# Kernel tuning notes

Hardware: AMD Instinct MI355X
Metric: run time of the kernel (lower is better)

## Reference

```python
import jax, jax.numpy as jnp
import numpy as np

COMPRESSION = 2  # max-pool factor along flattened spatial axis for phi and g


def setup_inputs() -> dict:
    key = jax.random.key(0)
    ks = jax.random.split(key, 5)
    B, C, H, W = 4, 64, 96, 96
    Ci = 32  # intermediate_dim = C // 2
    s = 1.0 / np.sqrt(C)
    return {
        "x": jax.random.normal(ks[0], (B, C, H, W), dtype=jnp.float32),
        "w_theta": jax.random.normal(ks[1], (Ci, C), dtype=jnp.float32) * s,
        "b_theta": jnp.zeros((Ci,), dtype=jnp.float32),
        "w_phi": jax.random.normal(ks[2], (Ci, C), dtype=jnp.float32) * s,
        "b_phi": jnp.zeros((Ci,), dtype=jnp.float32),
        "w_g": jax.random.normal(ks[3], (Ci, C), dtype=jnp.float32) * s,
        "b_g": jnp.zeros((Ci,), dtype=jnp.float32),
        "w_out": jax.random.normal(ks[4], (C, Ci), dtype=jnp.float32) * (1.0 / np.sqrt(Ci)),
        "b_out": jnp.zeros((C,), dtype=jnp.float32),
    }


def reference(x, w_theta, b_theta, w_phi, b_phi, w_g, b_g, w_out, b_out):
    B, C, H, W = x.shape
    N = H * W
    xf = x.reshape(B, C, N).transpose(0, 2, 1)            # [B, N, C]
    # 1x1 conv projections == channel matmuls
    theta = xf @ w_theta.T + b_theta                      # [B, N, Ci]
    phi = xf @ w_phi.T + b_phi                            # [B, N, Ci]
    g = xf @ w_g.T + b_g                                  # [B, N, Ci]
    # compression: max-pool (kernel=stride=COMPRESSION) along flattened spatial axis
    Ci = theta.shape[-1]
    phi = phi.reshape(B, N // COMPRESSION, COMPRESSION, Ci).max(axis=2)  # [B, N/c, Ci]
    g = g.reshape(B, N // COMPRESSION, COMPRESSION, Ci).max(axis=2)      # [B, N/c, Ci]
    # embedded-gaussian affinity + softmax
    attn = jax.nn.softmax(jnp.einsum('bnc,bmc->bnm', theta, phi), axis=-1)  # [B, N, N/c]
    y = jnp.einsum('bnm,bmc->bnc', attn, g)               # [B, N, Ci]
    out = y @ w_out.T + b_out                             # [B, N, C]
    out = out.transpose(0, 2, 1).reshape(B, C, H, W)
    return out + x  # residual
```

## Files before the change

### kernel.cpp

```cpp
#include <hip/hip_runtime.h>
#include <hip/hip_bf16.h>


#define NQ 9216
#define MM 4608
#define WM 1152
#define TPW 36
#define LOG2E 1.44269504088896340736f

typedef __attribute__((ext_vector_type(8))) short bf16x8;
typedef __attribute__((ext_vector_type(4))) float f32x4;
typedef __attribute__((ext_vector_type(4))) unsigned short u16x4;

static __device__ __forceinline__ unsigned pk2(float a, float b) {
    __hip_bfloat162 h = __float22bfloat162_rn(make_float2(a, b));
    return *reinterpret_cast<unsigned*>(&h);
}

__global__ __launch_bounds__(128, 4) void proj_kernel(
    const float* __restrict__ x,
    const float* __restrict__ wt, const float* __restrict__ bt,
    const float* __restrict__ wp, const float* __restrict__ bp,
    const float* __restrict__ wg, const float* __restrict__ bg,
    unsigned short* __restrict__ theta, unsigned short* __restrict__ phi,
    unsigned short* __restrict__ gT)
{
    __shared__ unsigned short gst[32 * 20];

    const int tid  = threadIdx.x;
    const int wid  = tid >> 6;
    const int lane = tid & 63;
    const int q = lane >> 4;
    const int c = lane & 15;

    const int b     = blockIdx.x / 288;
    const int rem   = blockIdx.x % 288;
    const int n0    = rem * 32 + wid * 16;

    const float* Wm[3] = {wt, wp, wg};
    const float* Bm[3] = {bt, bp, bg};

    bf16x8 wf[3][2][2];
    float bias[3][2];
#pragma unroll
    for (int p = 0; p < 3; ++p) {
#pragma unroll
        for (int ct = 0; ct < 2; ++ct) {
            bias[p][ct] = Bm[p][ct * 16 + c];
#pragma unroll
            for (int ks = 0; ks < 2; ++ks) {
                const float* wsrc = Wm[p] + (ct * 16 + c) * 64 + ks * 32 + q * 8;
                f32x4 w0 = *(const f32x4*)wsrc;
                f32x4 w1 = *(const f32x4*)(wsrc + 4);
                unsigned* wk = (unsigned*)&wf[p][ct][ks];
                wk[0] = pk2(w0[0], w0[1]); wk[1] = pk2(w0[2], w0[3]);
                wk[2] = pk2(w1[0], w1[1]); wk[3] = pk2(w1[2], w1[3]);
            }
        }
    }

    bf16x8 af[2];
#pragma unroll
    for (int ks = 0; ks < 2; ++ks) {
        unsigned* ap = (unsigned*)&af[ks];
#pragma unroll
        for (int j2 = 0; j2 < 4; ++j2) {
            float x0 = x[(b * 64 + ks * 32 + q * 8 + j2 * 2) * NQ + n0 + c];
            float x1 = x[(b * 64 + ks * 32 + q * 8 + j2 * 2 + 1) * NQ + n0 + c];
            ap[j2] = pk2(x0, x1);
        }
    }

#pragma unroll
    for (int p = 0; p < 3; ++p) {
#pragma unroll
        for (int ct = 0; ct < 2; ++ct) {
            f32x4 acc = {0.f, 0.f, 0.f, 0.f};
            acc = __builtin_amdgcn_mfma_f32_16x16x32_bf16(af[0], wf[p][ct][0], acc, 0, 0, 0);
            acc = __builtin_amdgcn_mfma_f32_16x16x32_bf16(af[1], wf[p][ct][1], acc, 0, 0, 0);
#pragma unroll
            for (int r = 0; r < 4; ++r) acc[r] += bias[p][ct];
            const int ci = ct * 16 + c;
            if (p == 0) {
                unsigned pv0 = pk2(acc[0] * LOG2E, acc[1] * LOG2E);
                unsigned pv1 = pk2(acc[2] * LOG2E, acc[3] * LOG2E);
                theta[(b * NQ + n0 + 4 * q + 0) * 32 + ci] = (unsigned short)pv0;
                theta[(b * NQ + n0 + 4 * q + 1) * 32 + ci] = (unsigned short)(pv0 >> 16);
                theta[(b * NQ + n0 + 4 * q + 2) * 32 + ci] = (unsigned short)pv1;
                theta[(b * NQ + n0 + 4 * q + 3) * 32 + ci] = (unsigned short)(pv1 >> 16);
            } else {
                unsigned pv = pk2(fmaxf(acc[0], acc[1]), fmaxf(acc[2], acc[3]));
                if (p == 1) {
                    const int m0 = (n0 >> 1) + 2 * q;
                    phi[(b * MM + m0) * 32 + ci]     = (unsigned short)pv;
                    phi[(b * MM + m0 + 1) * 32 + ci] = (unsigned short)(pv >> 16);
                } else {
                    *(unsigned int*)(gst + ci * 20 + wid * 8 + 2 * q) = pv;
                }
            }
        }
    }

    __syncthreads();
    {
        const int ci = tid >> 2;
        const int m4 = (tid & 3) * 4;
        u16x4 v = *(const u16x4*)(gst + ci * 20 + m4);
        *(u16x4*)(gT + (b * 32 + ci) * MM + rem * 16 + m4) = v;
    }
}

__global__ __launch_bounds__(256, 2) void attn_kernel(
    const unsigned short* __restrict__ theta, const unsigned short* __restrict__ phi,
    const unsigned short* __restrict__ gT,
    unsigned short* __restrict__ y)
{
    __shared__ unsigned short pld[4][64 * 32];
    __shared__ float red[4][64][36];
    __shared__ float lred[4][64];

    const int tid  = threadIdx.x;
    const int w    = tid >> 6;
    const int lane = tid & 63;
    const int q  = lane >> 4;
    const int c  = lane & 15;
    const int sw = ((c >> 1) & 3) << 3;

    const int b  = blockIdx.x / 144;
    const int nb = (blockIdx.x % 144) * 64;

    bf16x8 qf[4];
#pragma unroll
    for (int rt = 0; rt < 4; ++rt)
        qf[rt] = *(const bf16x8*)(theta + (b * NQ + nb + rt * 16 + c) * 32 + q * 8);

    const unsigned short* phiB = phi + (size_t)b * MM * 32;
    const unsigned short* gTB  = gT + (size_t)b * 32 * MM;
    unsigned short* myp = pld[w];

    f32x4 acc[4][2];
    float lsum[4];
#pragma unroll
    for (int rt = 0; rt < 4; ++rt) {
        lsum[rt] = 0.f;
#pragma unroll
        for (int s2 = 0; s2 < 2; ++s2) acc[rt][s2] = (f32x4){0.f, 0.f, 0.f, 0.f};
    }

    const int t0 = w * TPW;
    bf16x8 kf[2], vf[2];

#define LOAD_KF(m0) do {                                                      \
    kf[0] = *(const bf16x8*)(phiB + ((m0) + c) * 32 + q * 8);                 \
    kf[1] = *(const bf16x8*)(phiB + ((m0) + 16 + c) * 32 + q * 8);            \
} while (0)

#define LOAD_VF(m0) do {                                                      \
    vf[0] = *(const bf16x8*)(gTB + c * MM + (m0) + q * 8);                    \
    vf[1] = *(const bf16x8*)(gTB + (16 + c) * MM + (m0) + q * 8);             \
} while (0)

#define S_STEP(rt) do {                                                      \
    _Pragma("unroll")                                                        \
    for (int mct = 0; mct < 2; ++mct) {                                      \
        f32x4 z = {0.f, 0.f, 0.f, 0.f};                                      \
        f32x4 s = __builtin_amdgcn_mfma_f32_16x16x32_bf16(kf[mct], qf[rt], z, 0, 0, 0); \
        float e0 = __builtin_amdgcn_exp2f(s[0]);                             \
        float e1 = __builtin_amdgcn_exp2f(s[1]);                             \
        float e2 = __builtin_amdgcn_exp2f(s[2]);                             \
        float e3 = __builtin_amdgcn_exp2f(s[3]);                             \
        lsum[rt] += (e0 + e1) + (e2 + e3);                                   \
        uint2 hv = {pk2(e0, e1), pk2(e2, e3)};                               \
        *(uint2*)(myp + (((rt) * 16 + c) << 5) + ((mct * 16 + 4 * q) ^ sw)) = hv; \
    }                                                                        \
} while (0)

#define PV_STEP(rt) do {                                                     \
    bf16x8 pf = *(const bf16x8*)(myp + (((rt) * 16 + c) << 5) + ((q * 8) ^ sw)); \
    acc[rt][0] = __builtin_amdgcn_mfma_f32_16x16x32_bf16(vf[0], pf, acc[rt][0], 0, 0, 0); \
    acc[rt][1] = __builtin_amdgcn_mfma_f32_16x16x32_bf16(vf[1], pf, acc[rt][1], 0, 0, 0); \
} while (0)

    LOAD_KF(t0 * 32);
    LOAD_VF(t0 * 32);
    S_STEP(0); S_STEP(1); S_STEP(2); S_STEP(3);

    for (int mi = 1; mi < TPW; ++mi) {
        const int m0 = (t0 + mi) * 32;
        LOAD_KF(m0);
        PV_STEP(0); PV_STEP(1); PV_STEP(2); PV_STEP(3);
        LOAD_VF(m0);
        S_STEP(0); S_STEP(1); S_STEP(2); S_STEP(3);
    }

    PV_STEP(0); PV_STEP(1); PV_STEP(2); PV_STEP(3);

#undef LOAD_KF
#undef LOAD_VF
#undef S_STEP
#undef PV_STEP

#pragma unroll
    for (int rt = 0; rt < 4; ++rt) {
        float v = lsum[rt];
        v += __shfl_xor(v, 16);
        v += __shfl_xor(v, 32);
        if (lane < 16) lred[w][rt * 16 + lane] = v;
    }
#pragma unroll
    for (int rt = 0; rt < 4; ++rt)
#pragma unroll
        for (int s2 = 0; s2 < 2; ++s2)
            *(f32x4*)&red[w][rt * 16 + c][s2 * 16 + 4 * q] = acc[rt][s2];

    __syncthreads();

    {
        const int n   = tid & 63;
        const int cig = (tid >> 6) * 8;
        float ls = (lred[0][n] + lred[1][n]) + (lred[2][n] + lred[3][n]);
        float inv = 1.0f / ls;
        f32x4 s0 = {0.f, 0.f, 0.f, 0.f}, s1 = {0.f, 0.f, 0.f, 0.f};
#pragma unroll
        for (int ww = 0; ww < 4; ++ww) {
            s0 += *(const f32x4*)&red[ww][n][cig];
            s1 += *(const f32x4*)&red[ww][n][cig + 4];
        }
        unsigned short* yb = y + (size_t)(b * 32 + cig) * NQ + nb + n;
#pragma unroll
        for (int k = 0; k < 4; ++k) {
            yb[(size_t)k * NQ]       = (unsigned short)(pk2(s0[k] * inv, 0.f) & 0xffff);
            yb[(size_t)(k + 4) * NQ] = (unsigned short)(pk2(s1[k] * inv, 0.f) & 0xffff);
        }
    }
}

__global__ __launch_bounds__(128, 4) void oproj_kernel(
    const unsigned short* __restrict__ y,
    const float* __restrict__ w_out, const float* __restrict__ b_out,
    const float* __restrict__ x, float* __restrict__ out)
{
    __shared__ unsigned short yld[32 * 36];

    const int tid = threadIdx.x;
    const int b   = blockIdx.x / 288;
    const int nb  = (blockIdx.x % 288) * 32;

    {
        const int ci = tid >> 2;
        const int n8 = (tid & 3) * 8;
        const unsigned short* yr = y + (size_t)(b * 32 + ci) * NQ + nb + n8;
        uint2 v0 = *(const uint2*)yr;
        uint2 v1 = *(const uint2*)(yr + 4);
        *(uint2*)(yld + ci * 36 + n8)     = v0;
        *(uint2*)(yld + ci * 36 + n8 + 4) = v1;
    }
    __syncthreads();

    const int w    = tid >> 6;
    const int lane = tid & 63;
    const int q = lane >> 4;
    const int c = lane & 15;

    bf16x8 wof[4];
#pragma unroll
    for (int ct = 0; ct < 4; ++ct) {
        const float* wsrc = w_out + (ct * 16 + c) * 32 + q * 8;
        f32x4 w0 = *(const f32x4*)wsrc;
        f32x4 w1 = *(const f32x4*)(wsrc + 4);
        unsigned* wk = (unsigned*)&wof[ct];
        wk[0] = pk2(w0[0], w0[1]); wk[1] = pk2(w0[2], w0[3]);
        wk[2] = pk2(w1[0], w1[1]); wk[3] = pk2(w1[2], w1[3]);
    }

    bf16x8 yf;
    {
        unsigned short* yp = (unsigned short*)&yf;
#pragma unroll
        for (int j = 0; j < 8; ++j)
            yp[j] = yld[(q * 8 + j) * 36 + w * 16 + c];
    }

#pragma unroll
    for (int ct = 0; ct < 4; ++ct) {
        f32x4 z = {0.f, 0.f, 0.f, 0.f};
        f32x4 o = __builtin_amdgcn_mfma_f32_16x16x32_bf16(wof[ct], yf, z, 0, 0, 0);
#pragma unroll
        for (int r = 0; r < 4; ++r) {
            const int chn = ct * 16 + 4 * q + r;
            const size_t addr = (size_t)(b * 64 + chn) * NQ + nb + w * 16 + c;
            out[addr] = o[r] + b_out[chn] + x[addr];
        }
    }
}

extern "C" void kernel_launch(void* const* d_in, const int* in_sizes, int n_in,
                              void* d_out, int out_size, void* d_ws, size_t ws_size,
                              hipStream_t stream) {
    const float* x       = (const float*)d_in[0];
    const float* w_theta = (const float*)d_in[1];
    const float* b_theta = (const float*)d_in[2];
    const float* w_phi   = (const float*)d_in[3];
    const float* b_phi   = (const float*)d_in[4];
    const float* w_g     = (const float*)d_in[5];
    const float* b_g     = (const float*)d_in[6];
    const float* w_out   = (const float*)d_in[7];
    const float* b_out   = (const float*)d_in[8];
    float* out = (float*)d_out;

    unsigned short* theta = (unsigned short*)d_ws;
    unsigned short* phi   = theta + 4 * NQ * 32;
    unsigned short* gT    = phi + 4 * MM * 32;
    unsigned short* y     = gT + 4 * 32 * MM;

    proj_kernel<<<1152, 128, 0, stream>>>(x, w_theta, b_theta, w_phi, b_phi,
                                          w_g, b_g, theta, phi, gT);
    attn_kernel<<<576, 256, 0, stream>>>(theta, phi, gT, y);
    oproj_kernel<<<1152, 128, 0, stream>>>(y, w_out, b_out, x, out);
}
```

Before: 149.0 us.

## Fuse output projection into attention kernel and compute row sums via MFMA

The output-projection kernel is folded into the attention kernel's epilogue, so the bf16 y intermediate never goes through global memory and one launch is dropped. The query tile per block shrinks from 64 to 32 rows, giving 1152 blocks, and launch bounds rise to 5 blocks per SM for occupancy. Softmax denominators now come from an extra MFMA against a ones vector on the bf16 probabilities instead of VALU adds and shuffles. In exchange, each block reloads K/V for half as many queries, doubling K/V traffic per query, and each S/PV step gains an extra MFMA.

Measured after the change: 147.5 us. No clear change (-1.0%).

```diff
diff --git a/kernel.cpp b/kernel.cpp
--- a/kernel.cpp
+++ b/kernel.cpp
@@ -4,7 +4,6 @@
 
 #define NQ 9216
 #define MM 4608
-#define WM 1152
 #define TPW 36
 #define LOG2E 1.44269504088896340736f
 
@@ -110,14 +109,16 @@
     }
 }
 
-__global__ __launch_bounds__(256, 2) void attn_kernel(
+__global__ __launch_bounds__(256, 5) void attn_kernel(
     const unsigned short* __restrict__ theta, const unsigned short* __restrict__ phi,
     const unsigned short* __restrict__ gT,
-    unsigned short* __restrict__ y)
+    const float* __restrict__ w_out, const float* __restrict__ b_out,
+    const float* __restrict__ x, float* __restrict__ out)
 {
-    __shared__ unsigned short pld[4][64 * 32];
-    __shared__ float red[4][64][36];
-    __shared__ float lred[4][64];
+    __shared__ unsigned short pld[4][32 * 32];
+    __shared__ float red[4][32][36];
+    __shared__ float lred[4][32];
+    __shared__ unsigned short yld[32 * 34];
 
     const int tid  = threadIdx.x;
     const int w    = tid >> 6;
@@ -126,23 +127,30 @@
     const int c  = lane & 15;
     const int sw = ((c >> 1) & 3) << 3;
 
-    const int b  = blockIdx.x / 144;
-    const int nb = (blockIdx.x % 144) * 64;
-
-    bf16x8 qf[4];
-#pragma unroll
-    for (int rt = 0; rt < 4; ++rt)
+    const int b  = blockIdx.x / 288;
+    const int nb = (blockIdx.x % 288) * 32;
+
+    bf16x8 qf[2];
+#pragma unroll
+    for (int rt = 0; rt < 2; ++rt)
         qf[rt] = *(const bf16x8*)(theta + (b * NQ + nb + rt * 16 + c) * 32 + q * 8);
+
+    bf16x8 onef;
+    {
+        unsigned v = (c == 0) ? 0x3F803F80u : 0u;
+        unsigned* op = (unsigned*)&onef;
+        op[0] = v; op[1] = v; op[2] = v; op[3] = v;
+    }
 
     const unsigned short* phiB = phi + (size_t)b * MM * 32;
     const unsigned short* gTB  = gT + (size_t)b * 32 * MM;
     unsigned short* myp = pld[w];
 
-    f32x4 acc[4][2];
-    float lsum[4];
-#pragma unroll
-    for (int rt = 0; rt < 4; ++rt) {
-        lsum[rt] = 0.f;
+    f32x4 acc[2][2];
+    f32x4 lacc[2];
+#pragma unroll
+    for (int rt = 0; rt < 2; ++rt) {
+        lacc[rt] = (f32x4){0.f, 0.f, 0.f, 0.f};
 #pragma unroll
         for (int s2 = 0; s2 < 2; ++s2) acc[rt][s2] = (f32x4){0.f, 0.f, 0.f, 0.f};
     }
@@ -165,13 +173,9 @@
     for (int mct = 0; mct < 2; ++mct) {                                      \
         f32x4 z = {0.f, 0.f, 0.f, 0.f};                                      \
         f32x4 s = __builtin_amdgcn_mfma_f32_16x16x32_bf16(kf[mct], qf[rt], z, 0, 0, 0); \
-        float e0 = __builtin_amdgcn_exp2f(s[0]);                             \
-        float e1 = __builtin_amdgcn_exp2f(s[1]);                             \
-        float e2 = __builtin_amdgcn_exp2f(s[2]);                             \
-        float e3 = __builtin_amdgcn_exp2f(s[3]);                             \
-        lsum[rt] += (e0 + e1) + (e2 + e3);                                   \
-        uint2 hv = {pk2(e0, e1), pk2(e2, e3)};                               \
-        *(uint2*)(myp + (((rt) * 16 + c) << 5) + ((mct * 16 + 4 * q) ^ sw)) = hv; \
+        uint2 hv = {pk2(__builtin_amdgcn_exp2f(s[0]), __builtin_amdgcn_exp2f(s[1])),    \
+                    pk2(__builtin_amdgcn_exp2f(s[2]), __builtin_amdgcn_exp2f(s[3]))};   \
+        *(uint2*)(myp + (((rt) * 16 + c) << 5) + ((mct * 16 + 4 * q) ^ sw)) = hv;       \
     }                                                                        \
 } while (0)
 
@@ -179,36 +183,34 @@
     bf16x8 pf = *(const bf16x8*)(myp + (((rt) * 16 + c) << 5) + ((q * 8) ^ sw)); \
     acc[rt][0] = __builtin_amdgcn_mfma_f32_16x16x32_bf16(vf[0], pf, acc[rt][0], 0, 0, 0); \
     acc[rt][1] = __builtin_amdgcn_mfma_f32_16x16x32_bf16(vf[1], pf, acc[rt][1], 0, 0, 0); \
+    lacc[rt]   = __builtin_amdgcn_mfma_f32_16x16x32_bf16(onef,  pf, lacc[rt],   0, 0, 0); \
 } while (0)
 
     LOAD_KF(t0 * 32);
     LOAD_VF(t0 * 32);
-    S_STEP(0); S_STEP(1); S_STEP(2); S_STEP(3);
+    S_STEP(0); S_STEP(1);
 
     for (int mi = 1; mi < TPW; ++mi) {
         const int m0 = (t0 + mi) * 32;
         LOAD_KF(m0);
-        PV_STEP(0); PV_STEP(1); PV_STEP(2); PV_STEP(3);
+        PV_STEP(0); PV_STEP(1);
         LOAD_VF(m0);
-        S_STEP(0); S_STEP(1); S_STEP(2); S_STEP(3);
-    }
-
-    PV_STEP(0); PV_STEP(1); PV_STEP(2); PV_STEP(3);
+        S_STEP(0); S_STEP(1);
+    }
+
+    PV_STEP(0); PV_STEP(1);
 
 #undef LOAD_KF
 #undef LOAD_VF
 #undef S_STEP
 #undef PV_STEP
 
-#pragma unroll
-    for (int rt = 0; rt < 4; ++rt) {
-        float v = lsum[rt];
-        v += __shfl_xor(v, 16);
-        v += __shfl_xor(v, 32);
-        if (lane < 16) lred[w][rt * 16 + lane] = v;
-    }
-#pragma unroll
-    for (int rt = 0; rt < 4; ++rt)
+    if (lane < 16) {
+        lred[w][lane]      = lacc[0][0];
+        lred[w][16 + lane] = lacc[1][0];
+    }
+#pragma unroll
+    for (int rt = 0; rt < 2; ++rt)
 #pragma unroll
         for (int s2 = 0; s2 < 2; ++s2)
             *(f32x4*)&red[w][rt * 16 + c][s2 * 16 + 4 * q] = acc[rt][s2];
@@ -216,80 +218,45 @@
     __syncthreads();
 
     {
-        const int n   = tid & 63;
-        const int cig = (tid >> 6) * 8;
+        const int n  = tid & 31;
+        const int cg = (tid >> 5) * 4;
         float ls = (lred[0][n] + lred[1][n]) + (lred[2][n] + lred[3][n]);
         float inv = 1.0f / ls;
-        f32x4 s0 = {0.f, 0.f, 0.f, 0.f}, s1 = {0.f, 0.f, 0.f, 0.f};
-#pragma unroll
-        for (int ww = 0; ww < 4; ++ww) {
-            s0 += *(const f32x4*)&red[ww][n][cig];
-            s1 += *(const f32x4*)&red[ww][n][cig + 4];
-        }
-        unsigned short* yb = y + (size_t)(b * 32 + cig) * NQ + nb + n;
-#pragma unroll
-        for (int k = 0; k < 4; ++k) {
-            yb[(size_t)k * NQ]       = (unsigned short)(pk2(s0[k] * inv, 0.f) & 0xffff);
-            yb[(size_t)(k + 4) * NQ] = (unsigned short)(pk2(s1[k] * inv, 0.f) & 0xffff);
-        }
-    }
-}
-
-__global__ __launch_bounds__(128, 4) void oproj_kernel(
-    const unsigned short* __restrict__ y,
-    const float* __restrict__ w_out, const float* __restrict__ b_out,
-    const float* __restrict__ x, float* __restrict__ out)
-{
-    __shared__ unsigned short yld[32 * 36];
-
-    const int tid = threadIdx.x;
-    const int b   = blockIdx.x / 288;
-    const int nb  = (blockIdx.x % 288) * 32;
-
-    {
-        const int ci = tid >> 2;
-        const int n8 = (tid & 3) * 8;
-        const unsigned short* yr = y + (size_t)(b * 32 + ci) * NQ + nb + n8;
-        uint2 v0 = *(const uint2*)yr;
-        uint2 v1 = *(const uint2*)(yr + 4);
-        *(uint2*)(yld + ci * 36 + n8)     = v0;
-        *(uint2*)(yld + ci * 36 + n8 + 4) = v1;
+        f32x4 s = {0.f, 0.f, 0.f, 0.f};
+#pragma unroll
+        for (int ww = 0; ww < 4; ++ww)
+            s += *(const f32x4*)&red[ww][n][cg];
+#pragma unroll
+        for (int k = 0; k < 4; ++k)
+            yld[(cg + k) * 34 + n] = (unsigned short)(pk2(s[k] * inv, 0.f) & 0xffff);
     }
     __syncthreads();
 
-    const int w    = tid >> 6;
-    const int lane = tid & 63;
-    const int q = lane >> 4;
-    const int c = lane & 15;
-
-    bf16x8 wof[4];
-#pragma unroll
-    for (int ct = 0; ct < 4; ++ct) {
-        const float* wsrc = w_out + (ct * 16 + c) * 32 + q * 8;
-        f32x4 w0 = *(const f32x4*)wsrc;
-        f32x4 w1 = *(const f32x4*)(wsrc + 4);
-        unsigned* wk = (unsigned*)&wof[ct];
-        wk[0] = pk2(w0[0], w0[1]); wk[1] = pk2(w0[2], w0[3]);
-        wk[2] = pk2(w1[0], w1[1]); wk[3] = pk2(w1[2], w1[3]);
-    }
-
-    bf16x8 yf;
-    {
-        unsigned short* yp = (unsigned short*)&yf;
-#pragma unroll
-        for (int j = 0; j < 8; ++j)
-            yp[j] = yld[(q * 8 + j) * 36 + w * 16 + c];
-    }
-
-#pragma unroll
-    for (int ct = 0; ct < 4; ++ct) {
-        f32x4 z = {0.f, 0.f, 0.f, 0.f};
-        f32x4 o = __builtin_amdgcn_mfma_f32_16x16x32_bf16(wof[ct], yf, z, 0, 0, 0);
-#pragma unroll
-        for (int r = 0; r < 4; ++r) {
-            const int chn = ct * 16 + 4 * q + r;
-            const size_t addr = (size_t)(b * 64 + chn) * NQ + nb + w * 16 + c;
-            out[addr] = o[r] + b_out[chn] + x[addr];
+    {
+        bf16x8 wof;
+        {
+            const float* wsrc = w_out + (w * 16 + c) * 32 + q * 8;
+            f32x4 w0 = *(const f32x4*)wsrc;
+            f32x4 w1 = *(const f32x4*)(wsrc + 4);
+            unsigned* wk = (unsigned*)&wof;
+            wk[0] = pk2(w0[0], w0[1]); wk[1] = pk2(w0[2], w0[3]);
+            wk[2] = pk2(w1[0], w1[1]); wk[3] = pk2(w1[2], w1[3]);
+        }
+#pragma unroll
+        for (int nt = 0; nt < 2; ++nt) {
+            bf16x8 yf;
+            unsigned short* yp = (unsigned short*)&yf;
+#pragma unroll
+            for (int j = 0; j < 8; ++j)
+                yp[j] = yld[(q * 8 + j) * 34 + nt * 16 + c];
+            f32x4 z = {0.f, 0.f, 0.f, 0.f};
+            f32x4 o = __builtin_amdgcn_mfma_f32_16x16x32_bf16(wof, yf, z, 0, 0, 0);
+#pragma unroll
+            for (int r = 0; r < 4; ++r) {
+                const int chn = w * 16 + 4 * q + r;
+                const size_t addr = (size_t)(b * 64 + chn) * NQ + nb + nt * 16 + c;
+                out[addr] = o[r] + b_out[chn] + x[addr];
+            }
         }
     }
 }
@@ -311,10 +278,8 @@
     unsigned short* theta = (unsigned short*)d_ws;
     unsigned short* phi   = theta + 4 * NQ * 32;
     unsigned short* gT    = phi + 4 * MM * 32;
-    unsigned short* y     = gT + 4 * 32 * MM;
 
     proj_kernel<<<1152, 128, 0, stream>>>(x, w_theta, b_theta, w_phi, b_phi,
                                           w_g, b_g, theta, phi, gT);
-    attn_kernel<<<576, 256, 0, stream>>>(theta, phi, gT, y);
-    oproj_kernel<<<1152, 128, 0, stream>>>(y, w_out, b_out, x, out);
-}
+    attn_kernel<<<1152, 256, 0, stream>>>(theta, phi, gT, w_out, b_out, x, out);
+}
```
